# Kernel optimization log

Measured on AMD Instinct MI355X. Metric: run time of the kernel, lower is better.

## Reference

```python
import jax, jax.numpy as jnp
import numpy as np

B, S, E, D, H = 4, 1024, 1024, 1024, 16   # batch, dec_seq, enc_seq, d_model, n_heads
DH = D // H
DFF = 4096
EPS = 1e-5


def setup_inputs() -> dict:
    key = jax.random.key(0)
    ks = jax.random.split(key, 16)
    w = lambda k, shp: (jax.random.normal(k, shp, dtype=jnp.float32) * 0.02)
    return {
        "x": jax.random.normal(ks[0], (B, S, D), dtype=jnp.float32),
        "enc_x": jax.random.normal(ks[1], (B, E, D), dtype=jnp.float32),
        # masked self-attn (fused qkv)
        "w_qkv": w(ks[2], (D, 3 * D)), "b_qkv": jnp.zeros((3 * D,), jnp.float32),
        "w_sa_o": w(ks[3], (D, D)), "b_sa_o": jnp.zeros((D,), jnp.float32),
        # cross-attn
        "w_q": w(ks[4], (D, D)), "b_q": jnp.zeros((D,), jnp.float32),
        "w_k": w(ks[5], (D, D)), "b_k": jnp.zeros((D,), jnp.float32),
        "w_v": w(ks[6], (D, D)), "b_v": jnp.zeros((D,), jnp.float32),
        "w_ca_o": w(ks[7], (D, D)), "b_ca_o": jnp.zeros((D,), jnp.float32),
        # ffn
        "w1": w(ks[8], (D, DFF)), "b1": jnp.zeros((DFF,), jnp.float32),
        "w2": w(ks[9], (DFF, D)), "b2": jnp.zeros((D,), jnp.float32),
        # layernorms
        "g1": jnp.ones((D,), jnp.float32), "be1": jnp.zeros((D,), jnp.float32),
        "g2": jnp.ones((D,), jnp.float32), "be2": jnp.zeros((D,), jnp.float32),
        "g3": jnp.ones((D,), jnp.float32), "be3": jnp.zeros((D,), jnp.float32),
    }


def _layernorm(x, g, b):
    mean = jnp.mean(x, axis=-1, keepdims=True)
    var = jnp.mean(jnp.square(x - mean), axis=-1, keepdims=True)  # unbiased=False
    return g * (x - mean) / jnp.sqrt(var + EPS) + b


def _masked_self_attn(x, w_qkv, b_qkv, w_o, b_o):
    b, s, d = x.shape
    qkv = x @ w_qkv + b_qkv                            # [b,s,3D]
    # Faithful to torch: view as [b,s,H,3*DH] then chunk last dim (interleaved per-head).
    qkv = qkv.reshape(b, s, H, 3 * DH).transpose(0, 2, 1, 3)   # [b,H,s,3DH]
    q, k, v = jnp.split(qkv, 3, axis=-1)               # each [b,H,s,DH]
    scores = jnp.einsum('bhqd,bhkd->bhqk', q, k) / jnp.sqrt(jnp.float32(DH))
    mask = jnp.triu(jnp.ones((s, s), dtype=bool), k=1)
    scores = jnp.where(mask, -jnp.inf, scores)
    attn = jax.nn.softmax(scores, axis=-1)
    out = jnp.einsum('bhqk,bhkd->bhqd', attn, v)       # [b,H,s,DH]
    out = out.transpose(0, 2, 1, 3).reshape(b, s, d)
    return out @ w_o + b_o


def _cross_attn(dec_x, enc_x, w_q, b_q, w_k, b_k, w_v, b_v, w_o, b_o):
    b, sq, d = dec_x.shape
    sk = enc_x.shape[1]
    q = (dec_x @ w_q + b_q).reshape(b, sq, H, DH).transpose(0, 2, 1, 3)
    k = (enc_x @ w_k + b_k).reshape(b, sk, H, DH).transpose(0, 2, 1, 3)
    v = (enc_x @ w_v + b_v).reshape(b, sk, H, DH).transpose(0, 2, 1, 3)
    scores = jnp.einsum('bhqd,bhkd->bhqk', q, k) / jnp.sqrt(jnp.float32(DH))
    attn = jax.nn.softmax(scores, axis=-1)
    out = jnp.einsum('bhqk,bhkd->bhqd', attn, v).transpose(0, 2, 1, 3).reshape(b, sq, d)
    return out @ w_o + b_o


def reference(x, enc_x, w_qkv, b_qkv, w_sa_o, b_sa_o,
              w_q, b_q, w_k, b_k, w_v, b_v, w_ca_o, b_ca_o,
              w1, b1, w2, b2, g1, be1, g2, be2, g3, be3):
    h = _layernorm(x + _masked_self_attn(x, w_qkv, b_qkv, w_sa_o, b_sa_o), g1, be1)
    h = _layernorm(h + _cross_attn(h, enc_x, w_q, b_q, w_k, b_k, w_v, b_v, w_ca_o, b_ca_o), g2, be2)
    ffn = jax.nn.gelu(h @ w1 + b1, approximate=False) @ w2 + b2  # torch F.gelu default = exact
    return _layernorm(h + ffn, g3, be3)
```

## Files before the change

kernel.cpp:

```cpp
#include <hip/hip_runtime.h>

#define BB 4
#define SS 1024
#define DD 1024
#define HH 16
#define DHH 64
#define DFF 4096
#define MROWS 4096
#define NEG_BIG (-1e30f)
#define LOG2E 1.4426950408889634f
#define SCL_L2E 0.1803368801111244f

typedef float  f32x4  __attribute__((ext_vector_type(4)));
typedef __bf16 bf16x8 __attribute__((ext_vector_type(8)));
typedef __bf16 bf16x4 __attribute__((ext_vector_type(4)));

#define DEV __device__ __forceinline__

DEV void glds16(const __bf16* g, __bf16* l) {
  __builtin_amdgcn_global_load_lds((__attribute__((address_space(1))) void*)(g),
                                   (__attribute__((address_space(3))) void*)(l),
                                   16, 0, 0);
}

DEV float sanit(float v) {
  return fminf(fmaxf(v, -1e30f), 1e30f);
}

DEV float gelu_f(float v) {
  const float z  = fabsf(v) * 0.70710678118654752f;
  const float t  = __builtin_amdgcn_rcpf(1.f + 0.3275911f * z);
  float poly = ((((1.061405429f * t - 1.453152027f) * t + 1.421413741f) * t
                 - 0.284496736f) * t + 0.254829592f) * t;
  float er = 1.f - poly * __expf(-z * z);
  er = copysignf(er, v);
  return 0.5f * v * (1.f + er);
}

DEV void xcd_rowchunk(int& bx, int& by) {
  const int gx = gridDim.x;
  const int nwg = gx * gridDim.y;
  const int id = blockIdx.x + gx * blockIdx.y;
  const int idl = (id & 7) * (nwg >> 3) + (id >> 3);
  bx = idl % gx;
  by = idl / gx;
}

__global__ __launch_bounds__(256) void cvt_bf16(const float* __restrict__ src,
                                                __bf16* __restrict__ dst)
{
  const int idx = blockIdx.x * 256 + threadIdx.x;
  const f32x4 v = ((const f32x4*)src)[idx];
  bf16x4 o;
#pragma unroll
  for (int i = 0; i < 4; i++) o[i] = (__bf16)v[i];
  ((bf16x4*)dst)[idx] = o;
}

__global__ __launch_bounds__(256) void wtrans(const float* __restrict__ src,
                                              __bf16* __restrict__ dst,
                                              int K, int N)
{
  __shared__ float t[64][65];
  const int k0 = blockIdx.y * 64, n0 = blockIdx.x * 64;
  const int c = threadIdx.x & 63, r0 = threadIdx.x >> 6;
#pragma unroll
  for (int i = 0; i < 16; i++) {
    const int r = r0 * 16 + i;
    t[r][c] = src[(size_t)(k0 + r) * N + n0 + c];
  }
  __syncthreads();
#pragma unroll
  for (int i = 0; i < 16; i++) {
    const int r = r0 * 16 + i;
    dst[(size_t)(n0 + r) * K + k0 + c] = (__bf16)t[c][r];
  }
}

__global__ __launch_bounds__(256) void vtrans(const __bf16* __restrict__ src,
                                              int stride, int colMul, int colAdd,
                                              __bf16* __restrict__ dst)
{
  __shared__ __bf16 t[64][66];
  const int bh = blockIdx.y, b = bh >> 4, h = bh & 15;
  const int s0 = blockIdx.x * 64;
  const int c = threadIdx.x & 63, r0 = threadIdx.x >> 6;
  const __bf16* sp = src + (size_t)(b * SS) * stride + h * colMul + colAdd;
#pragma unroll
  for (int i = 0; i < 16; i++) {
    const int s = r0 * 16 + i;
    t[s][c] = sp[(size_t)(s0 + s) * stride + c];
  }
  __syncthreads();
  __bf16* dp = dst + (size_t)bh * 64 * 1024;
#pragma unroll
  for (int i = 0; i < 16; i++) {
    const int d = r0 * 16 + i;
    dp[(size_t)d * 1024 + s0 + c] = t[c][d];
  }
}

template<int MODE>
__global__ __launch_bounds__(256) void gemm_bt(
    const __bf16* __restrict__ A, const __bf16* __restrict__ Bt,
    const float* __restrict__ bias, const float* __restrict__ bias2,
    void* __restrict__ Cout, int N, int K)
{
  __shared__ __align__(16) __bf16 As[3][128 * 32];
  __shared__ __align__(16) __bf16 Bs[3][128 * 32];

  int bx, by;
  xcd_rowchunk(bx, by);
  const int bm = by * 128, bn = bx * 128;
  const int tid = threadIdx.x, wid = tid >> 6, lane = tid & 63;
  const int quad = lane >> 4, ln = lane & 15;

  const int sgc = ((lane & 3) ^ ((lane >> 3) & 3)) * 8;
  const __bf16* gA = A  + (size_t)(bm + wid * 32 + (lane >> 2)) * K + sgc;
  const __bf16* gB = Bt + (size_t)(bn + wid * 32 + (lane >> 2)) * K + sgc;
  const int soff = (wid * 32) * 32;
  const int qsw = (quad ^ ((ln >> 1) & 3)) * 8;

  f32x4 acc[4][4];
#pragma unroll
  for (int i = 0; i < 4; i++)
#pragma unroll
    for (int j = 0; j < 4; j++) acc[i][j] = (f32x4){0.f, 0.f, 0.f, 0.f};

  const int wr = (wid >> 1) * 64, wc = (wid & 1) * 64;

#define G_STAGE(buf, kt) do {                                     \
    const int k0_ = (kt) * 32;                                    \
    glds16(gA + k0_,          &As[buf][soff]);                    \
    glds16(gA + 16 * K + k0_, &As[buf][soff + 16 * 32]);          \
    glds16(gB + k0_,          &Bs[buf][soff]);                    \
    glds16(gB + 16 * K + k0_, &Bs[buf][soff + 16 * 32]);          \
  } while (0)

#define G_COMP(buf) do {                                                    \
    bf16x8 af[4], bfr[4];                                                   \
    _Pragma("unroll")                                                       \
    for (int i = 0; i < 4; i++)                                             \
      af[i] = *(const bf16x8*)(&As[buf][(wr + i * 16 + ln) * 32 + qsw]);    \
    _Pragma("unroll")                                                       \
    for (int j = 0; j < 4; j++)                                             \
      bfr[j] = *(const bf16x8*)(&Bs[buf][(wc + j * 16 + ln) * 32 + qsw]);   \
    _Pragma("unroll")                                                       \
    for (int i = 0; i < 4; i++)                                             \
      _Pragma("unroll")                                                     \
      for (int j = 0; j < 4; j++)                                           \
        acc[i][j] = __builtin_amdgcn_mfma_f32_16x16x32_bf16(af[i], bfr[j], acc[i][j], 0, 0, 0); \
  } while (0)

  const int nk = K >> 5;
  G_STAGE(0, 0); G_STAGE(1, 1); G_STAGE(2, 2);
  int cur = 0;
  for (int kt = 0; kt < nk; ++kt) {
    asm volatile("s_waitcnt vmcnt(8)" ::: "memory");
    __builtin_amdgcn_sched_barrier(0);
    __builtin_amdgcn_s_barrier();
    asm volatile("" ::: "memory");
    G_COMP(cur);
    __builtin_amdgcn_sched_barrier(0);
    asm volatile("" ::: "memory");
    __builtin_amdgcn_s_barrier();
    const int ks = (kt + 3 < nk) ? (kt + 3) : (nk - 1);
    G_STAGE(cur, ks);
    cur = (cur == 2) ? 0 : cur + 1;
  }
#undef G_STAGE
#undef G_COMP

#pragma unroll
  for (int j = 0; j < 4; j++) {
    const int col = bn + wc + j * 16 + ln;
    float bv;
    if (MODE == 4) bv = (col < 1024) ? bias[col] : bias2[col - 1024];
    else           bv = bias[col];
#pragma unroll
    for (int i = 0; i < 4; i++) {
#pragma unroll
      for (int r = 0; r < 4; r++) {
        const int row = bm + wr + i * 16 + quad * 4 + r;
        float v = sanit(acc[i][j][r] + bv);
        if (MODE == 1) v = gelu_f(v);
        if (MODE == 3 && (col % 192) < 64) v *= SCL_L2E;
        if (MODE == 2) ((float*)Cout)[(size_t)row * N + col] = v;
        else           ((__bf16*)Cout)[(size_t)row * N + col] = (__bf16)v;
      }
    }
  }
}

template<int MODE, int SPLIT>
__global__ __launch_bounds__(256) void gemm_bt64(
    const __bf16* __restrict__ A, const __bf16* __restrict__ Bt,
    const float* __restrict__ bias, void* __restrict__ Cout,
    int N, int K)
{
  __shared__ __align__(16) __bf16 As[3][128 * 32];
  __shared__ __align__(16) __bf16 Bs[3][64 * 32];

  int bx, by;
  xcd_rowchunk(bx, by);
  const int bm = by * 128, bn = bx * 64;
  const int kz = SPLIT ? blockIdx.z : 0;
  const int kOff = SPLIT ? kz * (K >> 1) : 0;
  const int tid = threadIdx.x, wid = tid >> 6, lane = tid & 63;
  const int quad = lane >> 4, ln = lane & 15;

  const int sgc = ((lane & 3) ^ ((lane >> 3) & 3)) * 8;
  const __bf16* gA = A  + (size_t)(bm + wid * 32 + (lane >> 2)) * K + sgc + kOff;
  const __bf16* gB = Bt + (size_t)(bn + wid * 16 + (lane >> 2)) * K + sgc + kOff;
  const int aoff = (wid * 32) * 32;
  const int boff = (wid * 16) * 32;
  const int qsw = (quad ^ ((ln >> 1) & 3)) * 8;

  f32x4 acc[4][2];
#pragma unroll
  for (int i = 0; i < 4; i++)
#pragma unroll
    for (int j = 0; j < 2; j++) acc[i][j] = (f32x4){0.f, 0.f, 0.f, 0.f};

  const int wr = (wid >> 1) * 64, wc = (wid & 1) * 32;

#define G_STAGE(buf, kt) do {                                     \
    const int k0_ = (kt) * 32;                                    \
    glds16(gA + k0_,          &As[buf][aoff]);                    \
    glds16(gA + 16 * K + k0_, &As[buf][aoff + 16 * 32]);          \
    glds16(gB + k0_,          &Bs[buf][boff]);                    \
  } while (0)

#define G_COMP(buf) do {                                                    \
    bf16x8 af[4], bfr[2];                                                   \
    _Pragma("unroll")                                                       \
    for (int i = 0; i < 4; i++)                                             \
      af[i] = *(const bf16x8*)(&As[buf][(wr + i * 16 + ln) * 32 + qsw]);    \
    _Pragma("unroll")                                                       \
    for (int j = 0; j < 2; j++)                                             \
      bfr[j] = *(const bf16x8*)(&Bs[buf][(wc + j * 16 + ln) * 32 + qsw]);   \
    _Pragma("unroll")                                                       \
    for (int i = 0; i < 4; i++)                                             \
      _Pragma("unroll")                                                     \
      for (int j = 0; j < 2; j++)                                           \
        acc[i][j] = __builtin_amdgcn_mfma_f32_16x16x32_bf16(af[i], bfr[j], acc[i][j], 0, 0, 0); \
  } while (0)

  const int nk = (K >> SPLIT) >> 5;
  G_STAGE(0, 0); G_STAGE(1, 1); G_STAGE(2, 2);
  int cur = 0;
  for (int kt = 0; kt < nk; ++kt) {
    asm volatile("s_waitcnt vmcnt(6)" ::: "memory");
    __builtin_amdgcn_sched_barrier(0);
    __builtin_amdgcn_s_barrier();
    asm volatile("" ::: "memory");
    G_COMP(cur);
    __builtin_amdgcn_sched_barrier(0);
    asm volatile("" ::: "memory");
    __builtin_amdgcn_s_barrier();
    const int ks = (kt + 3 < nk) ? (kt + 3) : (nk - 1);
    G_STAGE(cur, ks);
    cur = (cur == 2) ? 0 : cur + 1;
  }
#undef G_STAGE
#undef G_COMP

  float* outF = (float*)Cout + (SPLIT ? (size_t)kz * MROWS * N : 0);
#pragma unroll
  for (int j = 0; j < 2; j++) {
    const int col = bn + wc + j * 16 + ln;
    const float bv = (SPLIT && kz) ? 0.f : bias[col];
#pragma unroll
    for (int i = 0; i < 4; i++) {
#pragma unroll
      for (int r = 0; r < 4; r++) {
        const int row = bm + wr + i * 16 + quad * 4 + r;
        float v = sanit(acc[i][j][r] + bv);
        if (MODE == 3) v *= SCL_L2E;
        if (MODE == 2) outF[(size_t)row * N + col] = v;
        else           ((__bf16*)Cout)[(size_t)row * N + col] = (__bf16)v;
      }
    }
  }
}

__global__ __launch_bounds__(256) void attn(
    const __bf16* __restrict__ qp, int qStride, int qMul, int qAdd,
    const __bf16* __restrict__ kp, int kStride, int kMul, int kAdd,
    const __bf16* __restrict__ vt, __bf16* __restrict__ outp, int causal)
{
  __shared__ __align__(16) __bf16 Kt[2][64 * 64];
  __shared__ __align__(16) __bf16 Vt[2][64 * 64];
  __shared__ __align__(16) __bf16 ptl[4][32 * 64];

  const int id = blockIdx.x;
  const int bh = ((id >> 6) << 3) | (id & 7);
  const int q0 = (id >> 3) & 7;
  const int qblk = ((id >> 8) & 1) ? (7 - q0) : q0;
  const int b = bh >> 4, h = bh & 15;
  const int tid = threadIdx.x, wid = tid >> 6, lane = tid & 63;
  const int quad = lane >> 4, ln = lane & 15;
  const int qbase = qblk * 128;
  const int rowb0 = qbase + wid * 32;
  const int rowTop = rowb0 + 31;

  bf16x8 aq[2][2];
#pragma unroll
  for (int rf = 0; rf < 2; ++rf) {
    const __bf16* qr = qp + (size_t)(b * SS + rowb0 + rf * 16 + ln) * qStride
                          + h * qMul + qAdd;
#pragma unroll
    for (int ks = 0; ks < 2; ++ks)
      aq[rf][ks] = *(const bf16x8*)(qr + ks * 32 + quad * 8);
  }

  f32x4 acc[2][4];
#pragma unroll
  for (int rf = 0; rf < 2; ++rf)
#pragma unroll
    for (int nb = 0; nb < 4; ++nb) acc[rf][nb] = (f32x4){0.f, 0.f, 0.f, 0.f};
  float l_r[2][4] = {{0.f,0.f,0.f,0.f},{0.f,0.f,0.f,0.f}};

  const __bf16* kbase = kp + (size_t)(b * SS) * kStride + h * kMul + kAdd;
  const __bf16* vtb = vt + (size_t)bh * 64 * 1024;
  __bf16* ptw = ptl[wid];

  const int kvEnd = causal ? (qbase + 128) : SS;
  const int nT = kvEnd >> 6;

  const int sr = wid * 16 + (lane >> 3);
  const int sq = lane & 7;

#pragma unroll
  for (int p = 0; p < 2; ++p) {
    const int r = sr + p * 8;
    const int qs = (sq ^ (r & 7)) * 8;
    glds16(kbase + (size_t)r * kStride + qs, Kt[0] + (wid * 2 + p) * 512);
    glds16(vtb + (size_t)r * 1024 + qs,      Vt[0] + (wid * 2 + p) * 512);
  }

  for (int t = 0; t < nT; ++t) {
    const int cur = t & 1;
    const int kv0 = t * 64;

    if (t + 1 < nT) {
      const int kn = kv0 + 64;
#pragma unroll
      for (int p = 0; p < 2; ++p) {
        const int r = sr + p * 8;
        const int qs = (sq ^ (r & 7)) * 8;
        glds16(kbase + (size_t)(kn + r) * kStride + qs, Kt[cur ^ 1] + (wid * 2 + p) * 512);
        glds16(vtb + (size_t)r * 1024 + kn + qs,        Vt[cur ^ 1] + (wid * 2 + p) * 512);
      }
      __asm__ volatile("s_waitcnt vmcnt(4)" ::: "memory");
    } else {
      __asm__ volatile("s_waitcnt vmcnt(0)" ::: "memory");
    }
    __builtin_amdgcn_sched_barrier(0);
    __builtin_amdgcn_s_barrier();
    __asm__ volatile("" ::: "memory");
    __builtin_amdgcn_sched_barrier(0);

    if (!causal || kv0 <= rowTop) {
      const __bf16* kt = Kt[cur];
      const __bf16* vv = Vt[cur];

      f32x4 sc[2][4];
      {
        bf16x8 kf[4][2];
#pragma unroll
        for (int c = 0; c < 4; ++c) {
          const int row = c * 16 + ln;
#pragma unroll
          for (int ks = 0; ks < 2; ++ks)
            kf[c][ks] = *(const bf16x8*)(kt + row * 64 + (((ks * 4 + quad) ^ (ln & 7)) * 8));
        }
#pragma unroll
        for (int rf = 0; rf < 2; ++rf)
#pragma unroll
          for (int c = 0; c < 4; ++c) {
            f32x4 s_ = (f32x4){0.f, 0.f, 0.f, 0.f};
            s_ = __builtin_amdgcn_mfma_f32_16x16x32_bf16(aq[rf][0], kf[c][0], s_, 0, 0, 0);
            s_ = __builtin_amdgcn_mfma_f32_16x16x32_bf16(aq[rf][1], kf[c][1], s_, 0, 0, 0);
            sc[rf][c] = s_;
          }
      }

#pragma unroll
      for (int rf = 0; rf < 2; ++rf) {
        const bool doMask = causal && (kv0 + 63 > rowb0 + rf * 16);
#pragma unroll
        for (int r = 0; r < 4; ++r) {
          const int rowg = rowb0 + rf * 16 + quad * 4 + r;
          float p[4];
#pragma unroll
          for (int c = 0; c < 4; ++c) {
            float e = sc[rf][c][r];
            if (doMask && (kv0 + c * 16 + ln > rowg)) e = NEG_BIG;
            p[c] = exp2f(e);
          }
          l_r[rf][r] += (p[0] + p[1]) + (p[2] + p[3]);
          const int m = rf * 16 + quad * 4 + r;
          __bf16* pr = ptw + m * 64;
#pragma unroll
          for (int c = 0; c < 4; ++c) {
            const int col = c * 16 + ln;
            pr[(((col >> 3) ^ (m & 7)) << 3) + (col & 7)] = (__bf16)p[c];
          }
        }
      }
      __asm__ volatile("s_waitcnt lgkmcnt(0)" ::: "memory");
      __builtin_amdgcn_sched_barrier(0);

      {
        bf16x8 pa[2][2];
#pragma unroll
        for (int rf = 0; rf < 2; ++rf) {
          const int m = rf * 16 + ln;
#pragma unroll
          for (int ks = 0; ks < 2; ++ks)
            pa[rf][ks] = *(const bf16x8*)(ptw + m * 64 + (((ks * 4 + quad) ^ (m & 7)) * 8));
        }
#pragma unroll
        for (int nb = 0; nb < 4; ++nb) {
          const int vrow = nb * 16 + ln;
          const bf16x8 vf0 = *(const bf16x8*)(vv + vrow * 64 + (((quad)     ^ (ln & 7)) * 8));
          const bf16x8 vf1 = *(const bf16x8*)(vv + vrow * 64 + (((4 + quad) ^ (ln & 7)) * 8));
#pragma unroll
          for (int rf = 0; rf < 2; ++rf) {
            acc[rf][nb] = __builtin_amdgcn_mfma_f32_16x16x32_bf16(pa[rf][0], vf0, acc[rf][nb], 0, 0, 0);
            acc[rf][nb] = __builtin_amdgcn_mfma_f32_16x16x32_bf16(pa[rf][1], vf1, acc[rf][nb], 0, 0, 0);
          }
        }
      }
    }

    __asm__ volatile("" ::: "memory");
    __builtin_amdgcn_sched_barrier(0);
    __builtin_amdgcn_s_barrier();
  }

#pragma unroll
  for (int rf = 0; rf < 2; ++rf) {
#pragma unroll
    for (int r = 0; r < 4; ++r) {
      float l = l_r[rf][r];
#pragma unroll
      for (int off = 1; off < 16; off <<= 1) l += __shfl_xor(l, off, 64);
      const float inv = 1.f / fmaxf(l, 1e-30f);
      const int rowg = rowb0 + rf * 16 + quad * 4 + r;
      __bf16* op = outp + (size_t)(b * SS + rowg) * DD + h * 64;
#pragma unroll
      for (int nb = 0; nb < 4; ++nb)
        op[nb * 16 + ln] = (__bf16)sanit(acc[rf][nb][r] * inv);
    }
  }
}

__global__ __launch_bounds__(256) void ln_k(
    const float* __restrict__ residf, const float* __restrict__ proj,
    const float* __restrict__ proj2,
    const float* __restrict__ g, const float* __restrict__ be,
    float* __restrict__ outf, __bf16* __restrict__ outb)
{
  const int row = blockIdx.x, tid = threadIdx.x;
  const f32x4 pb = ((const f32x4*)(proj   + (size_t)row * 1024))[tid];
  const f32x4 rb = ((const f32x4*)(residf + (size_t)row * 1024))[tid];
  f32x4 x;
#pragma unroll
  for (int i = 0; i < 4; i++) x[i] = pb[i] + rb[i];
  if (proj2) {
    const f32x4 qb_ = ((const f32x4*)(proj2 + (size_t)row * 1024))[tid];
#pragma unroll
    for (int i = 0; i < 4; i++) x[i] += qb_[i];
  }
#pragma unroll
  for (int i = 0; i < 4; i++)
    x[i] = fminf(fmaxf(x[i], -1e15f), 1e15f);
  float s  = x[0] + x[1] + x[2] + x[3];
  float ss = x[0]*x[0] + x[1]*x[1] + x[2]*x[2] + x[3]*x[3];
#pragma unroll
  for (int off = 1; off < 64; off <<= 1) {
    s  += __shfl_xor(s,  off, 64);
    ss += __shfl_xor(ss, off, 64);
  }
  __shared__ float sm[8];
  if ((tid & 63) == 0) { sm[tid >> 6] = s; sm[4 + (tid >> 6)] = ss; }
  __syncthreads();
  s  = sm[0] + sm[1] + sm[2] + sm[3];
  ss = sm[4] + sm[5] + sm[6] + sm[7];
  const float mean = s * (1.f / 1024.f);
  const float var  = fmaxf(ss * (1.f / 1024.f) - mean * mean, 0.f);
  const float rstd = rsqrtf(var + 1e-5f);
  const int c = tid * 4;
  f32x4 o;
#pragma unroll
  for (int i = 0; i < 4; i++)
    o[i] = g[c + i] * ((x[i] - mean) * rstd) + be[c + i];
  if (outf) ((f32x4*)(outf + (size_t)row * 1024))[tid] = o;
  if (outb) {
    bf16x4 ob;
#pragma unroll
    for (int i = 0; i < 4; i++) ob[i] = (__bf16)o[i];
    ((bf16x4*)(outb + (size_t)row * 1024))[tid] = ob;
  }
}

extern "C" void kernel_launch(void* const* d_in, const int* in_sizes, int n_in,
                              void* d_out, int out_size, void* d_ws, size_t ws_size,
                              hipStream_t stream)
{
  const float* x      = (const float*)d_in[0];
  const float* enc    = (const float*)d_in[1];
  const float* w_qkv  = (const float*)d_in[2];
  const float* b_qkv  = (const float*)d_in[3];
  const float* w_sa_o = (const float*)d_in[4];
  const float* b_sa_o = (const float*)d_in[5];
  const float* w_q    = (const float*)d_in[6];
  const float* b_q    = (const float*)d_in[7];
  const float* w_k    = (const float*)d_in[8];
  const float* b_k    = (const float*)d_in[9];
  const float* w_v    = (const float*)d_in[10];
  const float* b_v    = (const float*)d_in[11];
  const float* w_ca_o = (const float*)d_in[12];
  const float* b_ca_o = (const float*)d_in[13];
  const float* w1     = (const float*)d_in[14];
  const float* b1     = (const float*)d_in[15];
  const float* w2     = (const float*)d_in[16];
  const float* b2     = (const float*)d_in[17];
  const float* g1     = (const float*)d_in[18];
  const float* be1    = (const float*)d_in[19];
  const float* g2     = (const float*)d_in[20];
  const float* be2    = (const float*)d_in[21];
  const float* g3     = (const float*)d_in[22];
  const float* be3    = (const float*)d_in[23];

  const size_t MB = 1024 * 1024;
  char* base = (char*)d_ws;
  __bf16* wqkvT = (__bf16*)(base + 0 * MB);
  __bf16* wsaoT = (__bf16*)(base + 6 * MB);
  __bf16* wqT   = (__bf16*)(base + 8 * MB);
  __bf16* wkvT  = (__bf16*)(base + 10 * MB);
  __bf16* wkT   = (__bf16*)(base + 10 * MB);
  __bf16* wvT   = (__bf16*)(base + 12 * MB);
  __bf16* wcaoT = (__bf16*)(base + 14 * MB);
  __bf16* w1T   = (__bf16*)(base + 0 * MB);
  __bf16* w2T   = (__bf16*)(base + 8 * MB);
  __bf16* xb    = (__bf16*)(base + 16 * MB);
  __bf16* encb  = (__bf16*)(base + 24 * MB);
  __bf16* qkv   = (__bf16*)(base + 32 * MB);
  __bf16* kvb   = (__bf16*)(base + 32 * MB);
  __bf16* qcab  = (__bf16*)(base + 48 * MB);
  __bf16* vt    = (__bf16*)(base + 56 * MB);
  __bf16* mid   = (__bf16*)(base + 32 * MB);
  __bf16* attnb = (__bf16*)(base + 64 * MB);
  float*  proj  = (float*) (base + 72 * MB);
  float*  h1f   = (float*) (base + 88 * MB);
  __bf16* h1b   = (__bf16*)(base + 104 * MB);
  float*  h2f   = (float*) (base + 112 * MB);
  __bf16* h2b   = (__bf16*)(base + 128 * MB);
  (void)wkT; (void)wvT;

  cvt_bf16<<<4096, 256, 0, stream>>>(x,   xb);
  cvt_bf16<<<4096, 256, 0, stream>>>(enc, encb);
  wtrans<<<dim3(48, 16), 256, 0, stream>>>(w_qkv,  wqkvT, 1024, 3072);
  wtrans<<<dim3(16, 16), 256, 0, stream>>>(w_sa_o, wsaoT, 1024, 1024);
  wtrans<<<dim3(16, 16), 256, 0, stream>>>(w_q,    wqT,   1024, 1024);
  wtrans<<<dim3(16, 16), 256, 0, stream>>>(w_k,    wkT,   1024, 1024);
  wtrans<<<dim3(16, 16), 256, 0, stream>>>(w_v,    wvT,   1024, 1024);
  wtrans<<<dim3(16, 16), 256, 0, stream>>>(w_ca_o, wcaoT, 1024, 1024);

  gemm_bt<3><<<dim3(24, 32), 256, 0, stream>>>(xb, wqkvT, b_qkv, nullptr, qkv, 3072, 1024);
  vtrans<<<dim3(16, 64), 256, 0, stream>>>(qkv, 3072, 192, 128, vt);
  attn<<<512, 256, 0, stream>>>(qkv, 3072, 192, 0,
                                qkv, 3072, 192, 64, vt, attnb, 1);
  gemm_bt64<2,0><<<dim3(16, 32), 256, 0, stream>>>(attnb, wsaoT, b_sa_o, proj, 1024, 1024);
  ln_k<<<4096, 256, 0, stream>>>(x, proj, nullptr, g1, be1, h1f, h1b);

  gemm_bt64<3,0><<<dim3(16, 32), 256, 0, stream>>>(h1b, wqT, b_q, qcab, 1024, 1024);
  gemm_bt<4><<<dim3(16, 32), 256, 0, stream>>>(encb, wkvT, b_k, b_v, kvb, 2048, 1024);
  vtrans<<<dim3(16, 64), 256, 0, stream>>>(kvb, 2048, 64, 1024, vt);
  attn<<<512, 256, 0, stream>>>(qcab, 1024, 64, 0,
                                kvb, 2048, 64, 0, vt, attnb, 0);
  gemm_bt64<2,0><<<dim3(16, 32), 256, 0, stream>>>(attnb, wcaoT, b_ca_o, proj, 1024, 1024);
  ln_k<<<4096, 256, 0, stream>>>(h1f, proj, nullptr, g2, be2, h2f, h2b);

  wtrans<<<dim3(64, 16), 256, 0, stream>>>(w1, w1T, 1024, 4096);
  wtrans<<<dim3(16, 64), 256, 0, stream>>>(w2, w2T, 4096, 1024);
  gemm_bt<1><<<dim3(32, 32), 256, 0, stream>>>(h2b, w1T, b1, nullptr, mid, 4096, 1024);
  gemm_bt64<2,1><<<dim3(16, 32, 2), 256, 0, stream>>>(mid, w2T, b2, proj, 1024, 4096);
  ln_k<<<4096, 256, 0, stream>>>(h2f, proj, proj + (size_t)MROWS * 1024,
                                 g3, be3, (float*)d_out, nullptr);

  (void)in_sizes; (void)n_in; (void)out_size; (void)ws_size;
}
```

Before: 541.1 us.

## Widen GEMM tiles to 128x256 and batch conversion/transpose launches

Replaces the 128x128 bf16 GEMM with a 128x256 tile variant (8 MFMA column fragments per wave, 64 B-rows staged per wave, waitcnt adjusted) for the QKV, KV and FFN1 projections, raising arithmetic intensity per loaded A tile. It also merges the two fp32->bf16 conversions into one launch and the five 1024x1024 weight transposes into a single kernel to reduce launch overhead. The larger tile doubles accumulator registers and LDS use, which may limit occupancy. It also halves the block count, so grids become small relative to the CU count, e.g. 256 blocks for the KV GEMM.

```diff
diff --git a/kernel.cpp b/kernel.cpp
--- a/kernel.cpp
+++ b/kernel.cpp
@@ -46,10 +46,14 @@
   by = idl / gx;
 }
 
-__global__ __launch_bounds__(256) void cvt_bf16(const float* __restrict__ src,
-                                                __bf16* __restrict__ dst)
-{
-  const int idx = blockIdx.x * 256 + threadIdx.x;
+__global__ __launch_bounds__(256) void cvt2_bf16(
+    const float* __restrict__ srcA, __bf16* __restrict__ dstA,
+    const float* __restrict__ srcB, __bf16* __restrict__ dstB)
+{
+  const int bid = blockIdx.x;
+  const float* src = (bid < 4096) ? srcA : srcB;
+  __bf16* dst      = (bid < 4096) ? dstA : dstB;
+  const int idx = ((bid < 4096) ? bid : (bid - 4096)) * 256 + threadIdx.x;
   const f32x4 v = ((const f32x4*)src)[idx];
   bf16x4 o;
 #pragma unroll
@@ -74,6 +78,35 @@
   for (int i = 0; i < 16; i++) {
     const int r = r0 * 16 + i;
     dst[(size_t)(n0 + r) * K + k0 + c] = (__bf16)t[c][r];
+  }
+}
+
+__global__ __launch_bounds__(256) void wtrans5(
+    const float* __restrict__ s0, const float* __restrict__ s1,
+    const float* __restrict__ s2, const float* __restrict__ s3,
+    const float* __restrict__ s4,
+    __bf16* __restrict__ d0, __bf16* __restrict__ d1,
+    __bf16* __restrict__ d2, __bf16* __restrict__ d3,
+    __bf16* __restrict__ d4)
+{
+  __shared__ float t[64][65];
+  const int wi = blockIdx.y >> 4;
+  const float* src = (wi == 0) ? s0 : (wi == 1) ? s1 : (wi == 2) ? s2
+                   : (wi == 3) ? s3 : s4;
+  __bf16* dst = (wi == 0) ? d0 : (wi == 1) ? d1 : (wi == 2) ? d2
+              : (wi == 3) ? d3 : d4;
+  const int k0 = (blockIdx.y & 15) * 64, n0 = blockIdx.x * 64;
+  const int c = threadIdx.x & 63, r0 = threadIdx.x >> 6;
+#pragma unroll
+  for (int i = 0; i < 16; i++) {
+    const int r = r0 * 16 + i;
+    t[r][c] = src[(size_t)(k0 + r) * 1024 + n0 + c];
+  }
+  __syncthreads();
+#pragma unroll
+  for (int i = 0; i < 16; i++) {
+    const int r = r0 * 16 + i;
+    dst[(size_t)(n0 + r) * 1024 + k0 + c] = (__bf16)t[c][r];
   }
 }
 
@@ -101,54 +134,57 @@
 }
 
 template<int MODE>
-__global__ __launch_bounds__(256) void gemm_bt(
+__global__ __launch_bounds__(256, 2) void gemm_bt256(
     const __bf16* __restrict__ A, const __bf16* __restrict__ Bt,
     const float* __restrict__ bias, const float* __restrict__ bias2,
     void* __restrict__ Cout, int N, int K)
 {
   __shared__ __align__(16) __bf16 As[3][128 * 32];
-  __shared__ __align__(16) __bf16 Bs[3][128 * 32];
+  __shared__ __align__(16) __bf16 Bs[3][256 * 32];
 
   int bx, by;
   xcd_rowchunk(bx, by);
-  const int bm = by * 128, bn = bx * 128;
+  const int bm = by * 128, bn = bx * 256;
   const int tid = threadIdx.x, wid = tid >> 6, lane = tid & 63;
   const int quad = lane >> 4, ln = lane & 15;
 
   const int sgc = ((lane & 3) ^ ((lane >> 3) & 3)) * 8;
   const __bf16* gA = A  + (size_t)(bm + wid * 32 + (lane >> 2)) * K + sgc;
-  const __bf16* gB = Bt + (size_t)(bn + wid * 32 + (lane >> 2)) * K + sgc;
-  const int soff = (wid * 32) * 32;
+  const __bf16* gB = Bt + (size_t)(bn + wid * 64 + (lane >> 2)) * K + sgc;
+  const int aoff = (wid * 32) * 32;
+  const int boff = (wid * 64) * 32;
   const int qsw = (quad ^ ((ln >> 1) & 3)) * 8;
 
-  f32x4 acc[4][4];
+  f32x4 acc[4][8];
 #pragma unroll
   for (int i = 0; i < 4; i++)
 #pragma unroll
-    for (int j = 0; j < 4; j++) acc[i][j] = (f32x4){0.f, 0.f, 0.f, 0.f};
-
-  const int wr = (wid >> 1) * 64, wc = (wid & 1) * 64;
+    for (int j = 0; j < 8; j++) acc[i][j] = (f32x4){0.f, 0.f, 0.f, 0.f};
+
+  const int wr = (wid >> 1) * 64, wc = (wid & 1) * 128;
 
 #define G_STAGE(buf, kt) do {                                     \
     const int k0_ = (kt) * 32;                                    \
-    glds16(gA + k0_,          &As[buf][soff]);                    \
-    glds16(gA + 16 * K + k0_, &As[buf][soff + 16 * 32]);          \
-    glds16(gB + k0_,          &Bs[buf][soff]);                    \
-    glds16(gB + 16 * K + k0_, &Bs[buf][soff + 16 * 32]);          \
+    glds16(gA + k0_,          &As[buf][aoff]);                    \
+    glds16(gA + 16 * K + k0_, &As[buf][aoff + 16 * 32]);          \
+    glds16(gB + k0_,          &Bs[buf][boff]);                    \
+    glds16(gB + 16 * K + k0_, &Bs[buf][boff + 16 * 32]);          \
+    glds16(gB + 32 * K + k0_, &Bs[buf][boff + 32 * 32]);          \
+    glds16(gB + 48 * K + k0_, &Bs[buf][boff + 48 * 32]);          \
   } while (0)
 
 #define G_COMP(buf) do {                                                    \
-    bf16x8 af[4], bfr[4];                                                   \
+    bf16x8 af[4], bfr[8];                                                   \
     _Pragma("unroll")                                                       \
     for (int i = 0; i < 4; i++)                                             \
       af[i] = *(const bf16x8*)(&As[buf][(wr + i * 16 + ln) * 32 + qsw]);    \
     _Pragma("unroll")                                                       \
-    for (int j = 0; j < 4; j++)                                             \
+    for (int j = 0; j < 8; j++)                                             \
       bfr[j] = *(const bf16x8*)(&Bs[buf][(wc + j * 16 + ln) * 32 + qsw]);   \
     _Pragma("unroll")                                                       \
     for (int i = 0; i < 4; i++)                                             \
       _Pragma("unroll")                                                     \
-      for (int j = 0; j < 4; j++)                                           \
+      for (int j = 0; j < 8; j++)                                           \
         acc[i][j] = __builtin_amdgcn_mfma_f32_16x16x32_bf16(af[i], bfr[j], acc[i][j], 0, 0, 0); \
   } while (0)
 
@@ -156,7 +192,7 @@
   G_STAGE(0, 0); G_STAGE(1, 1); G_STAGE(2, 2);
   int cur = 0;
   for (int kt = 0; kt < nk; ++kt) {
-    asm volatile("s_waitcnt vmcnt(8)" ::: "memory");
+    asm volatile("s_waitcnt vmcnt(12)" ::: "memory");
     __builtin_amdgcn_sched_barrier(0);
     __builtin_amdgcn_s_barrier();
     asm volatile("" ::: "memory");
@@ -172,7 +208,7 @@
 #undef G_COMP
 
 #pragma unroll
-  for (int j = 0; j < 4; j++) {
+  for (int j = 0; j < 8; j++) {
     const int col = bn + wc + j * 16 + ln;
     float bv;
     if (MODE == 4) bv = (col < 1024) ? bias[col] : bias2[col - 1024];
@@ -185,8 +221,7 @@
         float v = sanit(acc[i][j][r] + bv);
         if (MODE == 1) v = gelu_f(v);
         if (MODE == 3 && (col % 192) < 64) v *= SCL_L2E;
-        if (MODE == 2) ((float*)Cout)[(size_t)row * N + col] = v;
-        else           ((__bf16*)Cout)[(size_t)row * N + col] = (__bf16)v;
+        ((__bf16*)Cout)[(size_t)row * N + col] = (__bf16)v;
       }
     }
   }
@@ -561,16 +596,12 @@
   __bf16* h2b   = (__bf16*)(base + 128 * MB);
   (void)wkT; (void)wvT;
 
-  cvt_bf16<<<4096, 256, 0, stream>>>(x,   xb);
-  cvt_bf16<<<4096, 256, 0, stream>>>(enc, encb);
-  wtrans<<<dim3(48, 16), 256, 0, stream>>>(w_qkv,  wqkvT, 1024, 3072);
-  wtrans<<<dim3(16, 16), 256, 0, stream>>>(w_sa_o, wsaoT, 1024, 1024);
-  wtrans<<<dim3(16, 16), 256, 0, stream>>>(w_q,    wqT,   1024, 1024);
-  wtrans<<<dim3(16, 16), 256, 0, stream>>>(w_k,    wkT,   1024, 1024);
-  wtrans<<<dim3(16, 16), 256, 0, stream>>>(w_v,    wvT,   1024, 1024);
-  wtrans<<<dim3(16, 16), 256, 0, stream>>>(w_ca_o, wcaoT, 1024, 1024);
-
-  gemm_bt<3><<<dim3(24, 32), 256, 0, stream>>>(xb, wqkvT, b_qkv, nullptr, qkv, 3072, 1024);
+  cvt2_bf16<<<8192, 256, 0, stream>>>(x, xb, enc, encb);
+  wtrans<<<dim3(48, 16), 256, 0, stream>>>(w_qkv, wqkvT, 1024, 3072);
+  wtrans5<<<dim3(16, 80), 256, 0, stream>>>(w_sa_o, w_q, w_k, w_v, w_ca_o,
+                                            wsaoT, wqT, wkT, wvT, wcaoT);
+
+  gemm_bt256<3><<<dim3(12, 32), 256, 0, stream>>>(xb, wqkvT, b_qkv, nullptr, qkv, 3072, 1024);
   vtrans<<<dim3(16, 64), 256, 0, stream>>>(qkv, 3072, 192, 128, vt);
   attn<<<512, 256, 0, stream>>>(qkv, 3072, 192, 0,
                                 qkv, 3072, 192, 64, vt, attnb, 1);
@@ -578,7 +609,7 @@
   ln_k<<<4096, 256, 0, stream>>>(x, proj, nullptr, g1, be1, h1f, h1b);
 
   gemm_bt64<3,0><<<dim3(16, 32), 256, 0, stream>>>(h1b, wqT, b_q, qcab, 1024, 1024);
-  gemm_bt<4><<<dim3(16, 32), 256, 0, stream>>>(encb, wkvT, b_k, b_v, kvb, 2048, 1024);
+  gemm_bt256<4><<<dim3(8, 32), 256, 0, stream>>>(encb, wkvT, b_k, b_v, kvb, 2048, 1024);
   vtrans<<<dim3(16, 64), 256, 0, stream>>>(kvb, 2048, 64, 1024, vt);
   attn<<<512, 256, 0, stream>>>(qcab, 1024, 64, 0,
                                 kvb, 2048, 64, 0, vt, attnb, 0);
@@ -587,7 +618,7 @@
 
   wtrans<<<dim3(64, 16), 256, 0, stream>>>(w1, w1T, 1024, 4096);
   wtrans<<<dim3(16, 64), 256, 0, stream>>>(w2, w2T, 4096, 1024);
-  gemm_bt<1><<<dim3(32, 32), 256, 0, stream>>>(h2b, w1T, b1, nullptr, mid, 4096, 1024);
+  gemm_bt256<1><<<dim3(16, 32), 256, 0, stream>>>(h2b, w1T, b1, nullptr, mid, 4096, 1024);
   gemm_bt64<2,1><<<dim3(16, 32, 2), 256, 0, stream>>>(mid, w2T, b2, proj, 1024, 4096);
   ln_k<<<4096, 256, 0, stream>>>(h2f, proj, proj + (size_t)MROWS * 1024,
                                  g3, be3, (float*)d_out, nullptr);
```

New measurement: 538.6 us. About the same (-0.5%).
